# Kernel optimization log

Measured on AMD Instinct MI355X. Metric: run time of the kernel, lower is better.

The kernel has to match this reference:

```python
import jax, jax.numpy as jnp
import numpy as np

TEMPERATURE = 0.5


def setup_inputs() -> dict:
    key = jax.random.key(0)
    k1, k2 = jax.random.split(key)
    N, D = 4096, 256
    z_i = jax.random.normal(k1, (N, D), dtype=jnp.float32)
    z_j = jax.random.normal(k2, (N, D), dtype=jnp.float32)
    return {"z_i": z_i, "z_j": z_j}


def reference(z_i, z_j):
    N = z_i.shape[0]
    z = jnp.concatenate([z_i, z_j], axis=0)            # (2N, D)
    sim = (z @ z.T) / TEMPERATURE                       # (2N, 2N)
    # mask self-similarity on the diagonal
    diag = jnp.eye(2 * N, dtype=bool)
    sim = jnp.where(diag, -jnp.inf, sim)
    # positive pair labels: i <-> i+N
    labels = jnp.concatenate([jnp.arange(N, 2 * N), jnp.arange(0, N)])
    logp = jax.nn.log_softmax(sim, axis=-1)             # (2N, 2N)
    loss = -jnp.mean(jnp.take_along_axis(logp, labels[:, None], axis=-1))
    return loss
```

## Files before the change

kernel.cpp:

```cpp
#include <hip/hip_runtime.h>
#include <hip/hip_bf16.h>


typedef __bf16 bf16x8 __attribute__((ext_vector_type(8)));
typedef __bf16 bf16x4 __attribute__((ext_vector_type(4)));
typedef float  f32x16 __attribute__((ext_vector_type(16)));

#define NPAIR 4096
#define NROW  8192
#define DIM   256
#define STRIPS 16
#define RBLK  16384
#define SQSCALE 1.6986437f
#define LN2F    0.6931471805599453f
#define M2      176.0f

__global__ __launch_bounds__(256) void k_convert(const float* __restrict__ zi,
                                                 const float* __restrict__ zj,
                                                 __bf16* __restrict__ Zf,
                                                 float* __restrict__ pos,
                                                 float* __restrict__ out) {
    const int w = threadIdx.x >> 6, lane = threadIdx.x & 63;
    const int r = blockIdx.x * 4 + w;
    if (blockIdx.x == 0 && threadIdx.x == 0) out[0] = 0.0f;
    const float4 vi = *(const float4*)(zi + r * DIM + lane * 4);
    const float4 vj = *(const float4*)(zj + r * DIM + lane * 4);
    bf16x4 bi, bj;
    bi[0] = (__bf16)(vi.x * SQSCALE); bi[1] = (__bf16)(vi.y * SQSCALE);
    bi[2] = (__bf16)(vi.z * SQSCALE); bi[3] = (__bf16)(vi.w * SQSCALE);
    bj[0] = (__bf16)(vj.x * SQSCALE); bj[1] = (__bf16)(vj.y * SQSCALE);
    bj[2] = (__bf16)(vj.z * SQSCALE); bj[3] = (__bf16)(vj.w * SQSCALE);
    const int t = lane >> 2, h = (lane >> 1) & 1, inner = (lane & 1) * 8;
    char* Zb = (char*)Zf;
    *(bf16x4*)(Zb + (size_t)(r >> 5) * RBLK + t * 1024 + h * 512 + (r & 31) * 16 + inner) = bi;
    const int r2 = r + NPAIR;
    *(bf16x4*)(Zb + (size_t)(r2 >> 5) * RBLK + t * 1024 + h * 512 + (r2 & 31) * 16 + inner) = bj;
    float d = vi.x * vj.x + vi.y * vj.y + vi.z * vj.z + vi.w * vj.w;
    #pragma unroll
    for (int m = 32; m >= 1; m >>= 1) d += __shfl_xor(d, m);
    if (lane == 0) pos[r] = 2.0f * d;
}

__global__ __launch_bounds__(256, 2) void k_lse(const __bf16* __restrict__ Zf,
                                                float* __restrict__ Lpart) {
    const int bx    = blockIdx.x;
    const int rb    = bx & 31;
    const int strip = bx >> 5;
    const int tid   = threadIdx.x;
    const int w     = tid >> 6;
    const int lane  = tid & 63, lm = lane & 31, half = lane >> 5;
    const int laneoff = half * 512 + lm * 16;
    const int R0 = rb * 8 + w * 2, R1 = R0 + 1;

    __shared__ __align__(16) char smem[32768];
    const char* Zb = (const char*)Zf;

    bf16x8 B0[16], B1[16];
    {
        const char* g0 = Zb + (size_t)R0 * RBLK + laneoff;
        const char* g1 = Zb + (size_t)R1 * RBLK + laneoff;
        #pragma unroll
        for (int t = 0; t < 16; t++) {
            B0[t] = *(const bf16x8*)(g0 + t * 1024);
            B1[t] = *(const bf16x8*)(g1 + t * 1024);
        }
    }

    const char* Acol = Zb + (size_t)strip * 16 * RBLK;

    #define STAGE(bufsel, phidx) do {                                              \
        const char* _s = Acol + (size_t)(phidx) * RBLK + tid * 16;                 \
        char*       _d = smem + (bufsel) * 16384 + tid * 16;                       \
        _Pragma("unroll")                                                          \
        for (int _q = 0; _q < 4; _q++)                                             \
            __builtin_amdgcn_global_load_lds(                                      \
                (const __attribute__((address_space(1))) unsigned int*)(_s + _q * 4096), \
                (__attribute__((address_space(3))) unsigned int*)(_d + _q * 4096), \
                16, 0, 0);                                                         \
    } while (0)

    STAGE(0, 0);
    float l0 = 0.0f, l1 = 0.0f;

    #pragma unroll 2
    for (int ph = 0; ph < 16; ph++) {
        if (ph < 15) {
            STAGE((ph + 1) & 1, ph + 1);
            asm volatile("s_waitcnt vmcnt(4)" ::: "memory");
        } else {
            asm volatile("s_waitcnt vmcnt(0)" ::: "memory");
        }
        __builtin_amdgcn_s_barrier();
        __builtin_amdgcn_sched_barrier(0);

        const char* Ab = smem + (ph & 1) * 16384 + laneoff;
        f32x16 acc0 = (f32x16)(0.0f);
        f32x16 acc1 = (f32x16)(0.0f);
        __builtin_amdgcn_s_setprio(1);
        bf16x8 a = *(const bf16x8*)(Ab);
        #pragma unroll
        for (int t = 0; t < 16; t++) {
            bf16x8 na;
            if (t < 15) na = *(const bf16x8*)(Ab + (t + 1) * 1024);
            acc0 = __builtin_amdgcn_mfma_f32_32x32x16_bf16(a, B0[t], acc0, 0, 0, 0);
            acc1 = __builtin_amdgcn_mfma_f32_32x32x16_bf16(a, B1[t], acc1, 0, 0, 0);
            a = na;
        }
        __builtin_amdgcn_s_setprio(0);

        const int cb = strip * 16 + ph;
        float s0 = 0.0f, s1 = 0.0f;
        if (cb == R0) {
            #pragma unroll
            for (int rg = 0; rg < 16; rg++) {
                const int cl = (rg & 3) + 8 * (rg >> 2) + 4 * half;
                s0 += (cl == lm) ? 0.0f : __builtin_exp2f(acc0[rg] - M2);
            }
        } else {
            #pragma unroll
            for (int rg = 0; rg < 16; rg++) s0 += __builtin_exp2f(acc0[rg] - M2);
        }
        if (cb == R1) {
            #pragma unroll
            for (int rg = 0; rg < 16; rg++) {
                const int cl = (rg & 3) + 8 * (rg >> 2) + 4 * half;
                s1 += (cl == lm) ? 0.0f : __builtin_exp2f(acc1[rg] - M2);
            }
        } else {
            #pragma unroll
            for (int rg = 0; rg < 16; rg++) s1 += __builtin_exp2f(acc1[rg] - M2);
        }
        l0 += s0; l1 += s1;

        __builtin_amdgcn_sched_barrier(0);
        __builtin_amdgcn_s_barrier();
    }
    #undef STAGE

    l0 += __shfl_xor(l0, 32);
    l1 += __shfl_xor(l1, 32);
    if (half == 0) {
        Lpart[strip * NROW + R0 * 32 + lm] = l0;
        Lpart[strip * NROW + R1 * 32 + lm] = l1;
    }
}

__global__ __launch_bounds__(256) void k_final(const float* __restrict__ Lpart,
                                               const float* __restrict__ pos,
                                               float* __restrict__ out) {
    __shared__ float red[256];
    const int t = threadIdx.x;
    const int r = blockIdx.x * 256 + t;
    float l = 0.0f;
    #pragma unroll
    for (int s = 0; s < STRIPS; s++) l += Lpart[s * NROW + r];
    const float lse = (M2 + __builtin_log2f(l)) * LN2F;
    red[t] = lse - pos[r & (NPAIR - 1)];
    __syncthreads();
    for (int ofs = 128; ofs > 0; ofs >>= 1) {
        if (t < ofs) red[t] += red[t + ofs];
        __syncthreads();
    }
    if (t == 0) atomicAdd(out, red[0] / (float)NROW);
}

extern "C" void kernel_launch(void* const* d_in, const int* in_sizes, int n_in,
                              void* d_out, int out_size, void* d_ws, size_t ws_size,
                              hipStream_t stream) {
    const float* zi = (const float*)d_in[0];
    const float* zj = (const float*)d_in[1];
    __bf16* Zf   = (__bf16*)d_ws;
    float* pos   = (float*)((char*)d_ws + (size_t)NROW * DIM * 2);
    float* Lpart = pos + NPAIR;

    k_convert<<<NPAIR / 4, 256, 0, stream>>>(zi, zj, Zf, pos, (float*)d_out);
    k_lse<<<32 * STRIPS, 256, 0, stream>>>(Zf, Lpart);
    k_final<<<NROW / 256, 256, 0, stream>>>(Lpart, pos, (float*)d_out);
}
```

Baseline: 104.3 us.

## Software-pipeline exp2 reduction of previous tile under current tile's MFMAs

Defers each phase's exp2 accumulation to the next phase and interleaves those exp2 instructions between the MFMAs, so transcendental work overlaps matrix work instead of running serially after it. The diagonal is now masked by writing -1e30 into the accumulator rather than skipping terms. A drain loop after the main loop handles the last tile. It also deepens the LDS A-operand prefetch from one to four fragments, which raises register pressure in a kernel already holding 32 B-fragment registers per lane, and it moves the trailing barrier earlier.

New measurement: 103.9 us. Within noise of the previous version (-0.4%).

```diff
diff --git a/kernel.cpp b/kernel.cpp
--- a/kernel.cpp
+++ b/kernel.cpp
@@ -81,6 +81,8 @@
 
     STAGE(0, 0);
     float l0 = 0.0f, l1 = 0.0f;
+    f32x16 pacc0 = (f32x16)(-1e30f);
+    f32x16 pacc1 = (f32x16)(-1e30f);
 
     #pragma unroll 2
     for (int ph = 0; ph < 16; ph++) {
@@ -96,46 +98,55 @@
         const char* Ab = smem + (ph & 1) * 16384 + laneoff;
         f32x16 acc0 = (f32x16)(0.0f);
         f32x16 acc1 = (f32x16)(0.0f);
+
+        bf16x8 A[4];
+        #pragma unroll
+        for (int t = 0; t < 4; t++) A[t] = *(const bf16x8*)(Ab + t * 1024);
+
         __builtin_amdgcn_s_setprio(1);
-        bf16x8 a = *(const bf16x8*)(Ab);
         #pragma unroll
         for (int t = 0; t < 16; t++) {
-            bf16x8 na;
-            if (t < 15) na = *(const bf16x8*)(Ab + (t + 1) * 1024);
+            bf16x8 a = A[t & 3];
+            if (t < 12) A[t & 3] = *(const bf16x8*)(Ab + (t + 4) * 1024);
             acc0 = __builtin_amdgcn_mfma_f32_32x32x16_bf16(a, B0[t], acc0, 0, 0, 0);
             acc1 = __builtin_amdgcn_mfma_f32_32x32x16_bf16(a, B1[t], acc1, 0, 0, 0);
-            a = na;
+            if (t < 8) {
+                l0 += __builtin_exp2f(pacc0[2 * t]     - M2);
+                l0 += __builtin_exp2f(pacc0[2 * t + 1] - M2);
+            } else {
+                l1 += __builtin_exp2f(pacc1[2 * t - 16] - M2);
+                l1 += __builtin_exp2f(pacc1[2 * t - 15] - M2);
+            }
         }
         __builtin_amdgcn_s_setprio(0);
+        __builtin_amdgcn_sched_barrier(0);
+        __builtin_amdgcn_s_barrier();
 
         const int cb = strip * 16 + ph;
-        float s0 = 0.0f, s1 = 0.0f;
         if (cb == R0) {
             #pragma unroll
             for (int rg = 0; rg < 16; rg++) {
                 const int cl = (rg & 3) + 8 * (rg >> 2) + 4 * half;
-                s0 += (cl == lm) ? 0.0f : __builtin_exp2f(acc0[rg] - M2);
+                acc0[rg] = (cl == lm) ? -1e30f : acc0[rg];
             }
-        } else {
-            #pragma unroll
-            for (int rg = 0; rg < 16; rg++) s0 += __builtin_exp2f(acc0[rg] - M2);
         }
         if (cb == R1) {
             #pragma unroll
             for (int rg = 0; rg < 16; rg++) {
                 const int cl = (rg & 3) + 8 * (rg >> 2) + 4 * half;
-                s1 += (cl == lm) ? 0.0f : __builtin_exp2f(acc1[rg] - M2);
+                acc1[rg] = (cl == lm) ? -1e30f : acc1[rg];
             }
-        } else {
-            #pragma unroll
-            for (int rg = 0; rg < 16; rg++) s1 += __builtin_exp2f(acc1[rg] - M2);
         }
-        l0 += s0; l1 += s1;
-
-        __builtin_amdgcn_sched_barrier(0);
-        __builtin_amdgcn_s_barrier();
+        pacc0 = acc0;
+        pacc1 = acc1;
     }
     #undef STAGE
+
+    #pragma unroll
+    for (int rg = 0; rg < 16; rg++) {
+        l0 += __builtin_exp2f(pacc0[rg] - M2);
+        l1 += __builtin_exp2f(pacc1[rg] - M2);
+    }
 
     l0 += __shfl_xor(l0, 32);
     l1 += __shfl_xor(l1, 32);
```

## Deepen LDS staging to a four-buffer ring with one barrier per phase

Applied to the files above, without the earlier changes.

Replaces the double-buffered LDS staging of the A tiles with a four-slot ring (64KB). Three phases are prefetched ahead, and each new load is issued right after a single per-phase barrier, with vmcnt waits tuned to the number of loads still in flight. The diagonal mask now overwrites accumulator values with a large negative number instead of selecting a separate branch. The exp-sum reduction is split across independent accumulators, and inline asm pins the B fragments in registers. The intent is to hide more global-load latency and cut a barrier per phase, at the cost of more LDS per block, which may limit occupancy.

Result: faster. 100.5 us (-3.6%).

```diff
diff --git a/kernel.cpp b/kernel.cpp
--- a/kernel.cpp
+++ b/kernel.cpp
@@ -52,7 +52,7 @@
     const int laneoff = half * 512 + lm * 16;
     const int R0 = rb * 8 + w * 2, R1 = R0 + 1;
 
-    __shared__ __align__(16) char smem[32768];
+    __shared__ __align__(16) char smem[65536];
     const char* Zb = (const char*)Zf;
 
     bf16x8 B0[16], B1[16];
@@ -64,6 +64,11 @@
             B0[t] = *(const bf16x8*)(g0 + t * 1024);
             B1[t] = *(const bf16x8*)(g1 + t * 1024);
         }
+    }
+    #pragma unroll
+    for (int t = 0; t < 16; t++) {
+        asm volatile("" : "+v"(B0[t]));
+        asm volatile("" : "+v"(B1[t]));
     }
 
     const char* Acol = Zb + (size_t)strip * 16 * RBLK;
@@ -79,62 +84,62 @@
                 16, 0, 0);                                                         \
     } while (0)
 
-    STAGE(0, 0);
     float l0 = 0.0f, l1 = 0.0f;
 
-    #pragma unroll 2
-    for (int ph = 0; ph < 16; ph++) {
-        if (ph < 15) {
-            STAGE((ph + 1) & 1, ph + 1);
-            asm volatile("s_waitcnt vmcnt(4)" ::: "memory");
-        } else {
-            asm volatile("s_waitcnt vmcnt(0)" ::: "memory");
-        }
-        __builtin_amdgcn_s_barrier();
-        __builtin_amdgcn_sched_barrier(0);
+    #define PHASE_BODY(PH, WAITSTR, DO_STAGE) do {                                 \
+        asm volatile("s_waitcnt vmcnt(" WAITSTR ")" ::: "memory");                 \
+        __builtin_amdgcn_s_barrier();                                              \
+        asm volatile("" ::: "memory");                                             \
+        if (DO_STAGE) STAGE(((PH) + 3) & 3, (PH) + 3);                             \
+        const char* Ab = smem + ((PH) & 3) * 16384 + laneoff;                      \
+        f32x16 acc0 = (f32x16)(0.0f);                                              \
+        f32x16 acc1 = (f32x16)(0.0f);                                              \
+        __builtin_amdgcn_s_setprio(1);                                             \
+        _Pragma("unroll")                                                          \
+        for (int t = 0; t < 16; t++) {                                             \
+            bf16x8 a = *(const bf16x8*)(Ab + t * 1024);                            \
+            acc0 = __builtin_amdgcn_mfma_f32_32x32x16_bf16(a, B0[t], acc0, 0, 0, 0); \
+            acc1 = __builtin_amdgcn_mfma_f32_32x32x16_bf16(a, B1[t], acc1, 0, 0, 0); \
+        }                                                                          \
+        __builtin_amdgcn_s_setprio(0);                                             \
+        const int cb = strip * 16 + (PH);                                          \
+        if (cb == R0) {            \
+            _Pragma("unroll")                                                      \
+            for (int rg = 0; rg < 16; rg++) {                                      \
+                const int cl = (rg & 3) + 8 * (rg >> 2) + 4 * half;                \
+                acc0[rg] = (cl == lm) ? -1e30f : acc0[rg];                         \
+            }                                                                      \
+        }                                                                          \
+        if (cb == R1) {                                                            \
+            _Pragma("unroll")                                                      \
+            for (int rg = 0; rg < 16; rg++) {                                      \
+                const int cl = (rg & 3) + 8 * (rg >> 2) + 4 * half;                \
+                acc1[rg] = (cl == lm) ? -1e30f : acc1[rg];                         \
+            }                                                                      \
+        }                                                                          \
+        float p0 = 0.0f, p1 = 0.0f, q0 = 0.0f, q1 = 0.0f;                          \
+        _Pragma("unroll")                                                          \
+        for (int rg = 0; rg < 16; rg += 2) {                                       \
+            p0 += __builtin_exp2f(acc0[rg]     - M2);                              \
+            p1 += __builtin_exp2f(acc0[rg + 1] - M2);                              \
+            q0 += __builtin_exp2f(acc1[rg]     - M2);                              \
+            q1 += __builtin_exp2f(acc1[rg + 1] - M2);                              \
+        }                                                                          \
+        l0 += p0 + p1;                                                             \
+        l1 += q0 + q1;                                                             \
+    } while (0)
 
-        const char* Ab = smem + (ph & 1) * 16384 + laneoff;
-        f32x16 acc0 = (f32x16)(0.0f);
-        f32x16 acc1 = (f32x16)(0.0f);
-        __builtin_amdgcn_s_setprio(1);
-        bf16x8 a = *(const bf16x8*)(Ab);
-        #pragma unroll
-        for (int t = 0; t < 16; t++) {
-            bf16x8 na;
-            if (t < 15) na = *(const bf16x8*)(Ab + (t + 1) * 1024);
-            acc0 = __builtin_amdgcn_mfma_f32_32x32x16_bf16(a, B0[t], acc0, 0, 0, 0);
-            acc1 = __builtin_amdgcn_mfma_f32_32x32x16_bf16(a, B1[t], acc1, 0, 0, 0);
-            a = na;
-        }
-        __builtin_amdgcn_s_setprio(0);
+    STAGE(0, 0);
+    STAGE(1, 1);
+    STAGE(2, 2);
 
-        const int cb = strip * 16 + ph;
-        float s0 = 0.0f, s1 = 0.0f;
-        if (cb == R0) {
-            #pragma unroll
-            for (int rg = 0; rg < 16; rg++) {
-                const int cl = (rg & 3) + 8 * (rg >> 2) + 4 * half;
-                s0 += (cl == lm) ? 0.0f : __builtin_exp2f(acc0[rg] - M2);
-            }
-        } else {
-            #pragma unroll
-            for (int rg = 0; rg < 16; rg++) s0 += __builtin_exp2f(acc0[rg] - M2);
-        }
-        if (cb == R1) {
-            #pragma unroll
-            for (int rg = 0; rg < 16; rg++) {
-                const int cl = (rg & 3) + 8 * (rg >> 2) + 4 * half;
-                s1 += (cl == lm) ? 0.0f : __builtin_exp2f(acc1[rg] - M2);
-            }
-        } else {
-            #pragma unroll
-            for (int rg = 0; rg < 16; rg++) s1 += __builtin_exp2f(acc1[rg] - M2);
-        }
-        l0 += s0; l1 += s1;
+    for (int ph = 0; ph < 14; ph++) {
+        PHASE_BODY(ph, "8", ph < 13);
+    }
+    PHASE_BODY(14, "4", 0);
+    PHASE_BODY(15, "0", 0);
 
-        __builtin_amdgcn_sched_barrier(0);
-        __builtin_amdgcn_s_barrier();
-    }
+    #undef PHASE_BODY
     #undef STAGE
 
     l0 += __shfl_xor(l0, 32);
```

## Replace LDS-staged A tiles with direct global register loads in single-wave blocks

Applied to the files above, without the earlier changes.

The LSE kernel now launches one wave per block instead of four waves sharing a double-buffered LDS stage. Each wave streams its A operand straight from global memory into a 4-deep register ring, which removes the LDS staging and the block barriers. The diagonal is masked by overwriting accumulators before a branch-free exp2 sum that uses the raw hardware exp2 intrinsic and split partial sums. The cost is that each wave refetches the A tiles that four waves used to share, raising L2 and global traffic, and the shallow prefetch ring may leave load latency exposed.

Result: no change. 102.4 us (-1.8%).

```diff
diff --git a/kernel.cpp b/kernel.cpp
--- a/kernel.cpp
+++ b/kernel.cpp
@@ -14,6 +14,8 @@
 #define SQSCALE 1.6986437f
 #define LN2F    0.6931471805599453f
 #define M2      176.0f
+
+#define EXP2F(x) __builtin_amdgcn_exp2f(x)
 
 __global__ __launch_bounds__(256) void k_convert(const float* __restrict__ zi,
                                                  const float* __restrict__ zj,
@@ -41,101 +43,82 @@
     if (lane == 0) pos[r] = 2.0f * d;
 }
 
-__global__ __launch_bounds__(256, 2) void k_lse(const __bf16* __restrict__ Zf,
-                                                float* __restrict__ Lpart) {
-    const int bx    = blockIdx.x;
-    const int rb    = bx & 31;
-    const int strip = bx >> 5;
-    const int tid   = threadIdx.x;
-    const int w     = tid >> 6;
-    const int lane  = tid & 63, lm = lane & 31, half = lane >> 5;
+__global__ __launch_bounds__(64, 2) void k_lse(const __bf16* __restrict__ Zf,
+                                               float* __restrict__ Lpart) {
+    const int bid    = blockIdx.x;
+    const int strip  = bid >> 7;
+    const int rowblk = bid & 127;
+    const int lane = threadIdx.x & 63, lm = lane & 31, half = lane >> 5;
     const int laneoff = half * 512 + lm * 16;
-    const int R0 = rb * 8 + w * 2, R1 = R0 + 1;
+    const int R0 = rowblk * 2, R1 = R0 + 1;
 
-    __shared__ __align__(16) char smem[32768];
     const char* Zb = (const char*)Zf;
 
-    bf16x8 B0[16], B1[16];
-    {
-        const char* g0 = Zb + (size_t)R0 * RBLK + laneoff;
-        const char* g1 = Zb + (size_t)R1 * RBLK + laneoff;
-        #pragma unroll
-        for (int t = 0; t < 16; t++) {
-            B0[t] = *(const bf16x8*)(g0 + t * 1024);
-            B1[t] = *(const bf16x8*)(g1 + t * 1024);
-        }
+    const char* g0 = Zb + (size_t)R0 * RBLK + laneoff;
+    const char* g1 = Zb + (size_t)R1 * RBLK + laneoff;
+    #define LOADB(i) \
+        bf16x8 B0_##i = *(const bf16x8*)(g0 + (i) * 1024); \
+        bf16x8 B1_##i = *(const bf16x8*)(g1 + (i) * 1024);
+    LOADB(0)  LOADB(1)  LOADB(2)  LOADB(3)
+    LOADB(4)  LOADB(5)  LOADB(6)  LOADB(7)
+    LOADB(8)  LOADB(9)  LOADB(10) LOADB(11)
+    LOADB(12) LOADB(13) LOADB(14) LOADB(15)
+    #undef LOADB
+
+    const char* Ap = Zb + (size_t)strip * 16 * RBLK + laneoff;
+
+    bf16x8 A0 = *(const bf16x8*)(Ap + 0 * 1024);
+    bf16x8 A1 = *(const bf16x8*)(Ap + 1 * 1024);
+    bf16x8 A2 = *(const bf16x8*)(Ap + 2 * 1024);
+    bf16x8 A3 = *(const bf16x8*)(Ap + 3 * 1024);
+
+    float l0 = 0.0f, l1 = 0.0f;
+
+    #define RSTEP(i, RN) {                                                         \
+        bf16x8 a_ = RN;                                                            \
+        RN = *(const bf16x8*)(At + ((i) + 4) * 1024);                              \
+        acc0 = __builtin_amdgcn_mfma_f32_32x32x16_bf16(a_, B0_##i, acc0, 0, 0, 0); \
+        acc1 = __builtin_amdgcn_mfma_f32_32x32x16_bf16(a_, B1_##i, acc1, 0, 0, 0); \
     }
 
-    const char* Acol = Zb + (size_t)strip * 16 * RBLK;
-
-    #define STAGE(bufsel, phidx) do {                                              \
-        const char* _s = Acol + (size_t)(phidx) * RBLK + tid * 16;                 \
-        char*       _d = smem + (bufsel) * 16384 + tid * 16;                       \
-        _Pragma("unroll")                                                          \
-        for (int _q = 0; _q < 4; _q++)                                             \
-            __builtin_amdgcn_global_load_lds(                                      \
-                (const __attribute__((address_space(1))) unsigned int*)(_s + _q * 4096), \
-                (__attribute__((address_space(3))) unsigned int*)(_d + _q * 4096), \
-                16, 0, 0);                                                         \
-    } while (0)
-
-    STAGE(0, 0);
-    float l0 = 0.0f, l1 = 0.0f;
-
-    #pragma unroll 2
-    for (int ph = 0; ph < 16; ph++) {
-        if (ph < 15) {
-            STAGE((ph + 1) & 1, ph + 1);
-            asm volatile("s_waitcnt vmcnt(4)" ::: "memory");
-        } else {
-            asm volatile("s_waitcnt vmcnt(0)" ::: "memory");
-        }
-        __builtin_amdgcn_s_barrier();
-        __builtin_amdgcn_sched_barrier(0);
-
-        const char* Ab = smem + (ph & 1) * 16384 + laneoff;
+    for (int tile = 0; tile < 16; ++tile) {
+        const char* At = Ap + (size_t)tile * RBLK;
         f32x16 acc0 = (f32x16)(0.0f);
         f32x16 acc1 = (f32x16)(0.0f);
         __builtin_amdgcn_s_setprio(1);
-        bf16x8 a = *(const bf16x8*)(Ab);
-        #pragma unroll
-        for (int t = 0; t < 16; t++) {
-            bf16x8 na;
-            if (t < 15) na = *(const bf16x8*)(Ab + (t + 1) * 1024);
-            acc0 = __builtin_amdgcn_mfma_f32_32x32x16_bf16(a, B0[t], acc0, 0, 0, 0);
-            acc1 = __builtin_amdgcn_mfma_f32_32x32x16_bf16(a, B1[t], acc1, 0, 0, 0);
-            a = na;
-        }
+        RSTEP(0,  A0) RSTEP(1,  A1) RSTEP(2,  A2) RSTEP(3,  A3)
+        RSTEP(4,  A0) RSTEP(5,  A1) RSTEP(6,  A2) RSTEP(7,  A3)
+        RSTEP(8,  A0) RSTEP(9,  A1) RSTEP(10, A2) RSTEP(11, A3)
+        RSTEP(12, A0) RSTEP(13, A1) RSTEP(14, A2) RSTEP(15, A3)
         __builtin_amdgcn_s_setprio(0);
 
-        const int cb = strip * 16 + ph;
-        float s0 = 0.0f, s1 = 0.0f;
+        const int cb = strip * 16 + tile;
         if (cb == R0) {
             #pragma unroll
             for (int rg = 0; rg < 16; rg++) {
                 const int cl = (rg & 3) + 8 * (rg >> 2) + 4 * half;
-                s0 += (cl == lm) ? 0.0f : __builtin_exp2f(acc0[rg] - M2);
+                acc0[rg] = (cl == lm) ? -1e30f : acc0[rg];
             }
-        } else {
-            #pragma unroll
-            for (int rg = 0; rg < 16; rg++) s0 += __builtin_exp2f(acc0[rg] - M2);
         }
         if (cb == R1) {
             #pragma unroll
             for (int rg = 0; rg < 16; rg++) {
                 const int cl = (rg & 3) + 8 * (rg >> 2) + 4 * half;
-                s1 += (cl == lm) ? 0.0f : __builtin_exp2f(acc1[rg] - M2);
+                acc1[rg] = (cl == lm) ? -1e30f : acc1[rg];
             }
-        } else {
-            #pragma unroll
-            for (int rg = 0; rg < 16; rg++) s1 += __builtin_exp2f(acc1[rg] - M2);
         }
-        l0 += s0; l1 += s1;
-
-        __builtin_amdgcn_sched_barrier(0);
-        __builtin_amdgcn_s_barrier();
+        float p0 = 0.0f, p1 = 0.0f, q0 = 0.0f, q1 = 0.0f;
+        #pragma unroll
+        for (int rg = 0; rg < 16; rg += 2) {
+            p0 += EXP2F(acc0[rg]     - M2);
+            p1 += EXP2F(acc0[rg + 1] - M2);
+            q0 += EXP2F(acc1[rg]     - M2);
+            q1 += EXP2F(acc1[rg + 1] - M2);
+        }
+        l0 += p0 + p1;
+        l1 += q0 + q1;
     }
-    #undef STAGE
+    #undef RSTEP
 
     l0 += __shfl_xor(l0, 32);
     l1 += __shfl_xor(l1, 32);
@@ -174,6 +157,6 @@
     float* Lpart = pos + NPAIR;
 
     k_convert<<<NPAIR / 4, 256, 0, stream>>>(zi, zj, Zf, pos, (float*)d_out);
-    k_lse<<<32 * STRIPS, 256, 0, stream>>>(Zf, Lpart);
+    k_lse<<<128 * STRIPS, 64, 0, stream>>>(Zf, Lpart);
     k_final<<<NROW / 256, 256, 0, stream>>>(Lpart, pos, (float*)d_out);
 }
```
